# Kernel optimization log

Measured on AMD Instinct MI355X. Metric: run time of the kernel, lower is better.

## Reference

```python
import jax, jax.numpy as jnp
import numpy as np

N_NODES = 100000
D = 64


def sage_conv(x, src, dst, W_l, b_l, W_r, n_nodes):
    """PyG SAGEConv with mean aggregation and root_weight=True:
    out_i = lin_l(mean_{j in N(i)} x_j) + lin_r(x_i)
    Aggregation happens on raw features (as in PyG), then linear transforms.
    """
    deg = jax.ops.segment_sum(jnp.ones_like(dst, dtype=x.dtype), dst, num_segments=n_nodes)
    aggr = jax.ops.segment_sum(x[src], dst, num_segments=n_nodes)  # [N, D] gather-scatter
    aggr = aggr / jnp.maximum(deg, 1.0)[:, None]                    # mean (0 for isolated nodes)
    return aggr @ W_l.T + b_l + x @ W_r.T


def setup_inputs() -> dict:
    key = jax.random.key(0)
    k_x, k_e, k1, k2, k3, k4 = jax.random.split(key, 6)
    x = jax.random.normal(k_x, (N_NODES, D), dtype=jnp.float32)
    edge_index = jax.random.randint(k_e, (2, 1600000), 0, N_NODES, dtype=jnp.int64)
    s = 1.0 / np.sqrt(D)
    # layer 1 (SAGEConv: lin_l has bias, lin_r has no bias)
    W1_l = jax.random.uniform(k1, (D, D), jnp.float32, -s, s)
    b1_l = jnp.zeros((D,), jnp.float32)
    W1_r = jax.random.uniform(k2, (D, D), jnp.float32, -s, s)
    # layer 2
    W2_l = jax.random.uniform(k3, (D, D), jnp.float32, -s, s)
    b2_l = jnp.zeros((D,), jnp.float32)
    W2_r = jax.random.uniform(k4, (D, D), jnp.float32, -s, s)
    return {"x": x, "edge_index": edge_index,
            "W1_l": W1_l, "b1_l": b1_l, "W1_r": W1_r,
            "W2_l": W2_l, "b2_l": b2_l, "W2_r": W2_r}


def reference(x, edge_index, W1_l, b1_l, W1_r, W2_l, b2_l, W2_r):
    src, dst = edge_index[0], edge_index[1]
    n = x.shape[0]
    x1 = sage_conv(x, src, dst, W1_l, b1_l, W1_r, n)
    x2 = sage_conv(x1, src, dst, W2_l, b2_l, W2_r, n)
    return x2
```

## Files before the change

### kernel.cpp

```cpp
#include <hip/hip_runtime.h>

#define DD 64
#define BSHIFT 7
#define NBUCK_MAX 800
#define SEGCAP 4096
#define CBLK 512
#define SBLK 256

typedef unsigned short ushort_t;
typedef __attribute__((ext_vector_type(8))) short bf16x8;
typedef __attribute__((ext_vector_type(4))) short bf16x4;
typedef __attribute__((ext_vector_type(4))) float f32x4;

static __device__ __forceinline__ unsigned short f2bf(float f)
{
    unsigned u = __float_as_uint(f);
    unsigned r = (u + 0x7FFFu + ((u >> 16) & 1u)) >> 16;
    return (unsigned short)r;
}
static __device__ __forceinline__ float bf_lo(unsigned w) { return __uint_as_float(w << 16); }
static __device__ __forceinline__ float bf_hi(unsigned w) { return __uint_as_float(w & 0xFFFF0000u); }


__global__ __launch_bounds__(256)
void bucket_count(const int* __restrict__ dst, int* __restrict__ partialCnt,
                  int nE, int chunk, int nbuck)
{
    __shared__ int bins[NBUCK_MAX];
    int blk = blockIdx.x, t = threadIdx.x;
    for (int i = t; i < nbuck; i += 256) bins[i] = 0;
    __syncthreads();
    int e0 = blk * chunk;
    int e1 = e0 + chunk; if (e1 > nE) e1 = nE;
    for (int e = e0 + t; e < e1; e += 256)
        atomicAdd(&bins[dst[e] >> BSHIFT], 1);
    __syncthreads();
    for (int i = t; i < nbuck; i += 256)
        partialCnt[(size_t)i * CBLK + blk] = bins[i];
}

__global__ __launch_bounds__(CBLK)
void bucket_scanblocks(int* __restrict__ partialCnt, int* __restrict__ bucketTot)
{
    __shared__ int s[CBLK];
    int b = blockIdx.x, t = threadIdx.x;
    int v = partialCnt[(size_t)b * CBLK + t];
    s[t] = v;
    __syncthreads();
    for (int off = 1; off < CBLK; off <<= 1) {
        int u = (t >= off) ? s[t - off] : 0;
        __syncthreads();
        s[t] += u;
        __syncthreads();
    }
    partialCnt[(size_t)b * CBLK + t] = s[t] - v;
    if (t == CBLK - 1) bucketTot[b] = s[CBLK - 1];
}

__global__ __launch_bounds__(1024)
void bucket_scanbase(const int* __restrict__ bucketTot, int* __restrict__ bucketBase,
                     int* __restrict__ rs, int nbuck, int nN)
{
    __shared__ int s[1024];
    int t = threadIdx.x;
    int v = (t < nbuck) ? bucketTot[t] : 0;
    s[t] = v;
    __syncthreads();
    for (int off = 1; off < 1024; off <<= 1) {
        int u = (t >= off) ? s[t - off] : 0;
        __syncthreads();
        s[t] += u;
        __syncthreads();
    }
    if (t < nbuck) bucketBase[t] = s[t] - v;
    if (t == nbuck - 1) {
        bucketBase[nbuck] = s[t];
        rs[nN] = s[t];
    }
}

__global__ __launch_bounds__(256)
void bucket_scatter(const int* __restrict__ src, const int* __restrict__ dst,
                    const int* __restrict__ partialCnt,
                    const int* __restrict__ bucketBase,
                    int* __restrict__ buckEdges, int nE, int chunk, int nbuck)
{
    __shared__ int bins[NBUCK_MAX];
    __shared__ int wOff[NBUCK_MAX];
    int blk = blockIdx.x, t = threadIdx.x;
    for (int i = t; i < nbuck; i += 256) {
        bins[i] = 0;
        wOff[i] = bucketBase[i] + partialCnt[(size_t)i * CBLK + 2 * blk];
    }
    __syncthreads();
    int e0 = blk * chunk;
    int e1 = e0 + chunk; if (e1 > nE) e1 = nE;
    for (int e = e0 + t; e < e1; e += 256) {
        int d = dst[e];
        int sv = src[e];
        int bb = d >> BSHIFT;
        int r = atomicAdd(&bins[bb], 1);
        buckEdges[wOff[bb] + r] = sv | ((d & 127) << 17);
    }
}

__global__ __launch_bounds__(256)
void bucket_finalize(const int* __restrict__ buckEdges,
                     const int* __restrict__ bucketBase,
                     int* __restrict__ rs, int* __restrict__ csr,
                     float* __restrict__ indf, int nN)
{
    __shared__ int eLds[SEGCAP];
    __shared__ int segLds[SEGCAP];
    __shared__ int deg[128];
    __shared__ int basec[128];
    __shared__ int cur[128];
    int b = blockIdx.x, t = threadIdx.x;
    int e0 = bucketBase[b], e1 = bucketBase[b + 1];
    int nb = e1 - e0;
    bool staged = (nb <= SEGCAP);
    if (t < 128) deg[t] = 0;
    __syncthreads();
    for (int i = t; i < nb; i += 256) {
        int p = buckEdges[e0 + i];
        if (staged) eLds[i] = p;
        atomicAdd(&deg[(p >> 17) & 127], 1);
    }
    __syncthreads();
    if (t < 128) basec[t] = deg[t];
    __syncthreads();
    for (int off = 1; off < 128; off <<= 1) {
        int u = 0;
        if (t < 128 && t >= off) u = basec[t - off];
        __syncthreads();
        if (t < 128) basec[t] += u;
        __syncthreads();
    }
    int nodeBase = b << BSHIFT;
    if (t < 128) {
        int node = nodeBase + t;
        int ex = basec[t] - deg[t];
        if (node < nN) {
            rs[node] = e0 + ex;
            indf[node] = deg[t] > 0 ? 1.0f : 0.0f;
        }
        cur[t] = ex;
    }
    __syncthreads();
    for (int i = t; i < nb; i += 256) {
        int p = staged ? eLds[i] : buckEdges[e0 + i];
        int dl = (p >> 17) & 127;
        int slot = atomicAdd(&cur[dl], 1);
        int sv = p & 0x1FFFF;
        if (staged) segLds[slot] = sv;
        else        csr[e0 + slot] = sv;
    }
    __syncthreads();
    if (staged)
        for (int i = t; i < nb; i += 256)
            csr[e0 + i] = segLds[i];
}

__global__ __launch_bounds__(256)
void tobf16_kernel(const float* __restrict__ in, ushort_t* __restrict__ outh,
                   int nTot8)
{
    int i = blockIdx.x * 256 + threadIdx.x;
    if (i >= nTot8) return;
    float4 v0 = *(const float4*)(in + (size_t)i * 8);
    float4 v1 = *(const float4*)(in + (size_t)i * 8 + 4);
    uint4 o;
    o.x = (unsigned)f2bf(v0.x) | ((unsigned)f2bf(v0.y) << 16);
    o.y = (unsigned)f2bf(v0.z) | ((unsigned)f2bf(v0.w) << 16);
    o.z = (unsigned)f2bf(v1.x) | ((unsigned)f2bf(v1.y) << 16);
    o.w = (unsigned)f2bf(v1.z) | ((unsigned)f2bf(v1.w) << 16);
    *(uint4*)(outh + (size_t)i * 8) = o;
}

__global__ void prep_kernel(const float* __restrict__ W1l,
                            const float* __restrict__ W1r,
                            const float* __restrict__ W2l,
                            const float* __restrict__ W2r,
                            const float* __restrict__ b1,
                            const float* __restrict__ b2,
                            float* __restrict__ MT1, float* __restrict__ MT2,
                            float* __restrict__ MT3, float* __restrict__ c0,
                            float* __restrict__ c1)
{
    int f = blockIdx.x;
    int k = threadIdx.x;
    float m1 = 0.f, m2 = 0.f, m3 = 0.f;
    for (int j = 0; j < DD; ++j) {
        float a2l = W2l[f * DD + j];
        float a2r = W2r[f * DD + j];
        float w1l = W1l[j * DD + k];
        float w1r = W1r[j * DD + k];
        m1 = fmaf(a2l, w1l, m1);
        m2 = fmaf(a2l, w1r, m2);
        m2 = fmaf(a2r, w1l, m2);
        m3 = fmaf(a2r, w1r, m3);
    }
    MT1[k * DD + f] = m1;
    MT2[k * DD + f] = m2;
    MT3[k * DD + f] = m3;
    float t1 = W2l[f * DD + k] * b1[k];
    float t0 = W2r[f * DD + k] * b1[k];
    for (int off = 1; off < 64; off <<= 1) {
        t1 += __shfl_xor(t1, off);
        t0 += __shfl_xor(t0, off);
    }
    if (k == 0) {
        c1[f] = t1;
        c0[f] = t0 + b2[f];
    }
}

__global__ __launch_bounds__(256)
void pack_weights(const float* __restrict__ MT1, const float* __restrict__ MT2,
                  const float* __restrict__ MT3, ushort_t* __restrict__ Wp)
{
    int idx = blockIdx.x * 256 + threadIdx.x;
    if (idx >= 12288) return;
    int e    = idx & 7;
    int lane = (idx >> 3) & 63;
    int ft   = (idx >> 9) & 3;
    int kt   = (idx >> 11) & 1;
    int m    = idx >> 12;
    int kin  = ((lane >> 4) * 4) + (e & 3) + 16 * (e >> 2);
    int gk   = kt * 32 + kin;
    int f    = ft * 16 + (lane & 15);
    const float* MT = (m == 0) ? MT1 : (m == 1) ? MT2 : MT3;
    Wp[idx] = f2bf(MT[gk * DD + f]);
}

__global__ __launch_bounds__(256, 4)
void aggregate_bf16g(const ushort_t* __restrict__ xh,
                     const int* __restrict__ csr,
                     const int* __restrict__ rs,
                     ushort_t* __restrict__ aggrh, int nN)
{
    int lane = threadIdx.x & 63;
    int w = threadIdx.x >> 6;
    int g  = lane >> 3;
    int gl = lane & 7;
    int node = (blockIdx.x * 4 + w) * 8 + g;
    int valid = node < nN;
    int nd = valid ? node : nN - 1;
    int beg = rs[nd], end = rs[nd + 1];
    int deg = end - beg;

    float4 aL0 = {0,0,0,0}, aH0 = {0,0,0,0};
    float4 aL1 = {0,0,0,0}, aH1 = {0,0,0,0};
    float4 aL2 = {0,0,0,0}, aH2 = {0,0,0,0};
    float4 aL3 = {0,0,0,0}, aH3 = {0,0,0,0};

#define ROWA(S, L, H)                                                         \
    {                                                                         \
        uint4 v = *(const uint4*)(xh + (size_t)(S) * DD + gl * 8);            \
        L.x += bf_lo(v.x); L.y += bf_hi(v.x);                                 \
        L.z += bf_lo(v.y); L.w += bf_hi(v.y);                                 \
        H.x += bf_lo(v.z); H.y += bf_hi(v.z);                                 \
        H.z += bf_lo(v.w); H.w += bf_hi(v.w);                                 \
    }
#define ROWM(S, MM, L, H)                                                     \
    {                                                                         \
        uint4 v = *(const uint4*)(xh + (size_t)(S) * DD + gl * 8);            \
        L.x = fmaf(MM, bf_lo(v.x), L.x); L.y = fmaf(MM, bf_hi(v.x), L.y);     \
        L.z = fmaf(MM, bf_lo(v.y), L.z); L.w = fmaf(MM, bf_hi(v.y), L.w);     \
        H.x = fmaf(MM, bf_lo(v.z), H.x); H.y = fmaf(MM, bf_hi(v.z), H.y);     \
        H.z = fmaf(MM, bf_lo(v.w), H.z); H.w = fmaf(MM, bf_hi(v.w), H.w);     \
    }

    for (int ch = 0; ch < deg; ch += 8) {
        int ii = ch + gl;
        int myIdx = csr[(ii < deg) ? (beg + ii) : beg];
        int lb = g << 3;
        if (ch + 8 <= deg) {
            int s0 = __shfl(myIdx, lb + 0);
            int s1 = __shfl(myIdx, lb + 1);
            int s2 = __shfl(myIdx, lb + 2);
            int s3 = __shfl(myIdx, lb + 3);
            ROWA(s0, aL0, aH0) ROWA(s1, aL1, aH1)
            ROWA(s2, aL2, aH2) ROWA(s3, aL3, aH3)
            int s4 = __shfl(myIdx, lb + 4);
            int s5 = __shfl(myIdx, lb + 5);
            int s6 = __shfl(myIdx, lb + 6);
            int s7 = __shfl(myIdx, lb + 7);
            ROWA(s4, aL0, aH0) ROWA(s5, aL1, aH1)
            ROWA(s6, aL2, aH2) ROWA(s7, aL3, aH3)
        } else {
            int rem = deg - ch;
            int s0 = __shfl(myIdx, lb + 0);
            int s1 = __shfl(myIdx, lb + 1);
            int s2 = __shfl(myIdx, lb + 2);
            int s3 = __shfl(myIdx, lb + 3);
            float m0 = (0 < rem) ? 1.f : 0.f;
            float m1 = (1 < rem) ? 1.f : 0.f;
            float m2 = (2 < rem) ? 1.f : 0.f;
            float m3 = (3 < rem) ? 1.f : 0.f;
            ROWM(s0, m0, aL0, aH0) ROWM(s1, m1, aL1, aH1)
            ROWM(s2, m2, aL2, aH2) ROWM(s3, m3, aL3, aH3)
            int s4 = __shfl(myIdx, lb + 4);
            int s5 = __shfl(myIdx, lb + 5);
            int s6 = __shfl(myIdx, lb + 6);
            int s7 = __shfl(myIdx, lb + 7);
            float m4 = (4 < rem) ? 1.f : 0.f;
            float m5 = (5 < rem) ? 1.f : 0.f;
            float m6 = (6 < rem) ? 1.f : 0.f;
            float m7 = (7 < rem) ? 1.f : 0.f;
            ROWM(s4, m4, aL0, aH0) ROWM(s5, m5, aL1, aH1)
            ROWM(s6, m6, aL2, aH2) ROWM(s7, m7, aL3, aH3)
        }
    }
#undef ROWA
#undef ROWM

    float4 L, H;
    L.x = (aL0.x + aL1.x) + (aL2.x + aL3.x);
    L.y = (aL0.y + aL1.y) + (aL2.y + aL3.y);
    L.z = (aL0.z + aL1.z) + (aL2.z + aL3.z);
    L.w = (aL0.w + aL1.w) + (aL2.w + aL3.w);
    H.x = (aH0.x + aH1.x) + (aH2.x + aH3.x);
    H.y = (aH0.y + aH1.y) + (aH2.y + aH3.y);
    H.z = (aH0.z + aH1.z) + (aH2.z + aH3.z);
    H.w = (aH0.w + aH1.w) + (aH2.w + aH3.w);
    if (valid) {
        float inv = 1.0f / (float)(deg > 0 ? deg : 1);
        uint4 o;
        o.x = (unsigned)f2bf(L.x * inv) | ((unsigned)f2bf(L.y * inv) << 16);
        o.y = (unsigned)f2bf(L.z * inv) | ((unsigned)f2bf(L.w * inv) << 16);
        o.z = (unsigned)f2bf(H.x * inv) | ((unsigned)f2bf(H.y * inv) << 16);
        o.w = (unsigned)f2bf(H.z * inv) | ((unsigned)f2bf(H.w * inv) << 16);
        *(uint4*)(aggrh + (size_t)node * DD + gl * 8) = o;
    }
}

__global__ __launch_bounds__(256)
void tri_dense_mfma(const ushort_t* __restrict__ agg2h,
                    const ushort_t* __restrict__ agg1h,
                    const ushort_t* __restrict__ xh,
                    const ushort_t* __restrict__ Wp,
                    const float* __restrict__ c0,
                    const float* __restrict__ c1,
                    const float* __restrict__ indf,
                    float* __restrict__ out, int nN)
{
    int lane = threadIdx.x & 63;
    int w = threadIdx.x >> 6;
    int base = (blockIdx.x * 4 + w) * 16;
    if (base >= nN) return;
    int mrow = lane & 15;
    int kg   = lane >> 4;
    size_t rowoff = (size_t)(base + mrow) * DD + kg * 4;

    bf16x4 aLo[3][2], aHi[3][2];
#pragma unroll
    for (int m = 0; m < 3; ++m) {
        const ushort_t* sp = (m == 0) ? agg2h : (m == 1) ? agg1h : xh;
#pragma unroll
        for (int kt = 0; kt < 2; ++kt) {
            aLo[m][kt] = *(const bf16x4*)(sp + rowoff + kt * 32);
            aHi[m][kt] = *(const bf16x4*)(sp + rowoff + kt * 32 + 16);
        }
    }
    float ind0 = indf[base + kg * 4 + 0];
    float ind1 = indf[base + kg * 4 + 1];
    float ind2 = indf[base + kg * 4 + 2];
    float ind3 = indf[base + kg * 4 + 3];
    float c0v[4], c1v[4];
#pragma unroll
    for (int ft = 0; ft < 4; ++ft) {
        c0v[ft] = c0[ft * 16 + mrow];
        c1v[ft] = c1[ft * 16 + mrow];
    }

    f32x4 acc0 = {0,0,0,0}, acc1 = {0,0,0,0}, acc2 = {0,0,0,0}, acc3 = {0,0,0,0};
#pragma unroll
    for (int m = 0; m < 3; ++m) {
#pragma unroll
        for (int kt = 0; kt < 2; ++kt) {
            bf16x8 a;
            a[0] = aLo[m][kt][0]; a[1] = aLo[m][kt][1];
            a[2] = aLo[m][kt][2]; a[3] = aLo[m][kt][3];
            a[4] = aHi[m][kt][0]; a[5] = aHi[m][kt][1];
            a[6] = aHi[m][kt][2]; a[7] = aHi[m][kt][3];
            const ushort_t* wp = Wp + ((m * 2 + kt) * 4) * 512 + lane * 8;
            bf16x8 b0 = *(const bf16x8*)(wp);
            bf16x8 b1 = *(const bf16x8*)(wp + 512);
            bf16x8 b2 = *(const bf16x8*)(wp + 1024);
            bf16x8 b3 = *(const bf16x8*)(wp + 1536);
            acc0 = __builtin_amdgcn_mfma_f32_16x16x32_bf16(a, b0, acc0, 0, 0, 0);
            acc1 = __builtin_amdgcn_mfma_f32_16x16x32_bf16(a, b1, acc1, 0, 0, 0);
            acc2 = __builtin_amdgcn_mfma_f32_16x16x32_bf16(a, b2, acc2, 0, 0, 0);
            acc3 = __builtin_amdgcn_mfma_f32_16x16x32_bf16(a, b3, acc3, 0, 0, 0);
        }
    }

#define STORE_T(ACC, ft)                                                      \
    {                                                                         \
        int f = (ft) * 16 + mrow;                                             \
        size_t o = (size_t)(base + kg * 4) * DD + f;                          \
        out[o         ] = ACC[0] + c0v[ft] + ind0 * c1v[ft];                  \
        out[o + DD    ] = ACC[1] + c0v[ft] + ind1 * c1v[ft];                  \
        out[o + 2 * DD] = ACC[2] + c0v[ft] + ind2 * c1v[ft];                  \
        out[o + 3 * DD] = ACC[3] + c0v[ft] + ind3 * c1v[ft];                  \
    }
    STORE_T(acc0, 0) STORE_T(acc1, 1) STORE_T(acc2, 2) STORE_T(acc3, 3)
#undef STORE_T
}

extern "C" void kernel_launch(void* const* d_in, const int* in_sizes, int n_in,
                              void* d_out, int out_size, void* d_ws, size_t ws_size,
                              hipStream_t stream)
{
    const float* x   = (const float*)d_in[0];
    const int*   ei  = (const int*)d_in[1];
    const float* W1l = (const float*)d_in[2];
    const float* b1l = (const float*)d_in[3];
    const float* W1r = (const float*)d_in[4];
    const float* W2l = (const float*)d_in[5];
    const float* b2l = (const float*)d_in[6];
    const float* W2r = (const float*)d_in[7];
    float* out = (float*)d_out;

    int nN = in_sizes[0] / DD;
    int nE = in_sizes[1] / 2;
    const int* src = ei;
    const int* dst = ei + nE;

    int nbuck = (nN + 127) >> BSHIFT;
    int cchunk = (nE + CBLK - 1) / CBLK;
    int schunk = cchunk * 2;

    int* rs         = (int*)d_ws;
    int* partialCnt = rs + nN + 1;
    int* bucketTot  = partialCnt + (size_t)nbuck * CBLK;
    int* bucketBase = bucketTot + nbuck;
    int* csr        = bucketBase + nbuck + 1;
    int* buckEdges  = csr + nE;
    size_t ofs = (size_t)(buckEdges + nE - (int*)d_ws);
    ofs = (ofs + 3) & ~(size_t)3;
    float* MT1 = (float*)d_ws + ofs;
    float* MT2 = MT1 + DD * DD;
    float* MT3 = MT2 + DD * DD;
    float* c0 = MT3 + DD * DD;
    float* c1 = c0 + DD;
    float* xh_f    = c1 + DD;
    float* agg1h_f = xh_f + (size_t)nN * 32;
    float* agg2h_f = agg1h_f + (size_t)nN * 32;
    float* indf    = agg2h_f + (size_t)nN * 32;
    ushort_t* Wp   = (ushort_t*)(indf + nN);
    ushort_t* xh    = (ushort_t*)xh_f;
    ushort_t* agg1h = (ushort_t*)agg1h_f;
    ushort_t* agg2h = (ushort_t*)agg2h_f;

    int ncv  = (nN * 32 / 4 + 255) / 256;
    int nagg = (nN + 31) / 32;
    int nmf  = (nN / 16 + 3) / 4;

    bucket_count<<<CBLK, 256, 0, stream>>>(dst, partialCnt, nE, cchunk, nbuck);
    bucket_scanblocks<<<nbuck, CBLK, 0, stream>>>(partialCnt, bucketTot);
    bucket_scanbase<<<1, 1024, 0, stream>>>(bucketTot, bucketBase, rs, nbuck, nN);
    bucket_scatter<<<SBLK, 256, 0, stream>>>(src, dst, partialCnt, bucketBase,
                                             buckEdges, nE, schunk, nbuck);
    bucket_finalize<<<nbuck, 256, 0, stream>>>(buckEdges, bucketBase, rs, csr,
                                               indf, nN);

    prep_kernel<<<64, 64, 0, stream>>>(W1l, W1r, W2l, W2r, b1l, b2l,
                                       MT1, MT2, MT3, c0, c1);
    pack_weights<<<48, 256, 0, stream>>>(MT1, MT2, MT3, Wp);
    tobf16_kernel<<<ncv, 256, 0, stream>>>(x, xh, nN * DD / 8);

    aggregate_bf16g<<<nagg, 256, 0, stream>>>(xh, csr, rs, agg1h, nN);
    aggregate_bf16g<<<nagg, 256, 0, stream>>>(agg1h, csr, rs, agg2h, nN);

    tri_dense_mfma<<<nmf, 256, 0, stream>>>(agg2h, agg1h, xh, Wp,
                                            c0, c1, indf, out, nN);
}
```

Measured before the change: 141.7 us.

## Gather neighbor features in FP8 instead of BF16 for both aggregations

Node features are quantized to 8-bit floats before the edge gathers. Both aggregation passes now read 64-byte rows instead of 128-byte rows, roughly halving the random gather traffic. The first aggregation writes an FP8 copy alongside its BF16 output for the second pass to gather from. The dense MFMA stage reads the original fp32 x and converts it to BF16 in registers instead of using a BF16 copy. The cost is lower feature precision in the aggregated means, which risks accuracy against the fp32 reference, plus extra pack and convert work.

```diff
diff --git a/kernel.cpp b/kernel.cpp
--- a/kernel.cpp
+++ b/kernel.cpp
@@ -8,9 +8,20 @@
 #define SBLK 256
 
 typedef unsigned short ushort_t;
+typedef unsigned char uchar_t;
 typedef __attribute__((ext_vector_type(8))) short bf16x8;
 typedef __attribute__((ext_vector_type(4))) short bf16x4;
 typedef __attribute__((ext_vector_type(4))) float f32x4;
+typedef __attribute__((ext_vector_type(2))) float f32x2;
+
+#if defined(__has_builtin)
+#if __has_builtin(__builtin_amdgcn_cvt_pk_f32_fp8) && __has_builtin(__builtin_amdgcn_cvt_pk_fp8_f32)
+#define HW_FP8 1
+#endif
+#endif
+#ifndef HW_FP8
+#define HW_FP8 0
+#endif
 
 static __device__ __forceinline__ unsigned short f2bf(float f)
 {
@@ -20,6 +31,43 @@
 }
 static __device__ __forceinline__ float bf_lo(unsigned w) { return __uint_as_float(w << 16); }
 static __device__ __forceinline__ float bf_hi(unsigned w) { return __uint_as_float(w & 0xFFFF0000u); }
+
+static __device__ __forceinline__ unsigned f2q8_sw(float f)
+{
+    unsigned u = __float_as_uint(f);
+    unsigned s = (u >> 31) << 7;
+    unsigned um = __float_as_uint(__uint_as_float(u & 0x7FFFFFFFu) * 0x1.0p-120f);
+    unsigned q = (um + 0x7FFFFu + ((um >> 20) & 1u)) >> 20;
+    if (q > 0x7Eu) q = 0x7Eu;
+    return s | q;
+}
+static __device__ __forceinline__ float q2f_sw(unsigned b)
+{
+    unsigned u = ((b & 0x80u) << 24) | ((b & 0x7Fu) << 20);
+    return __uint_as_float(u) * 0x1.0p120f;
+}
+template<int WORD>
+static __device__ __forceinline__ f32x2 cvt2(unsigned u)
+{
+#if HW_FP8
+    return __builtin_amdgcn_cvt_pk_f32_fp8(u, WORD);
+#else
+    unsigned b0 = (u >> (WORD * 16)) & 0xFFu;
+    unsigned b1 = (u >> (WORD * 16 + 8)) & 0xFFu;
+    f32x2 r; r[0] = q2f_sw(b0); r[1] = q2f_sw(b1);
+    return r;
+#endif
+}
+template<int WORD>
+static __device__ __forceinline__ unsigned pk8(float x, float y, unsigned old)
+{
+#if HW_FP8
+    return __builtin_amdgcn_cvt_pk_fp8_f32(x, y, old, WORD);
+#else
+    unsigned q = f2q8_sw(x) | (f2q8_sw(y) << 8);
+    return WORD ? ((old & 0x0000FFFFu) | (q << 16)) : ((old & 0xFFFF0000u) | q);
+#endif
+}
 
 
 __global__ __launch_bounds__(256)
@@ -162,19 +210,19 @@
 }
 
 __global__ __launch_bounds__(256)
-void tobf16_kernel(const float* __restrict__ in, ushort_t* __restrict__ outh,
-                   int nTot8)
+void tofp8_kernel(const float* __restrict__ in, uchar_t* __restrict__ outq,
+                  int nTot8)
 {
     int i = blockIdx.x * 256 + threadIdx.x;
     if (i >= nTot8) return;
     float4 v0 = *(const float4*)(in + (size_t)i * 8);
     float4 v1 = *(const float4*)(in + (size_t)i * 8 + 4);
-    uint4 o;
-    o.x = (unsigned)f2bf(v0.x) | ((unsigned)f2bf(v0.y) << 16);
-    o.y = (unsigned)f2bf(v0.z) | ((unsigned)f2bf(v0.w) << 16);
-    o.z = (unsigned)f2bf(v1.x) | ((unsigned)f2bf(v1.y) << 16);
-    o.w = (unsigned)f2bf(v1.z) | ((unsigned)f2bf(v1.w) << 16);
-    *(uint4*)(outh + (size_t)i * 8) = o;
+    unsigned w0 = pk8<0>(v0.x, v0.y, 0u);
+    w0 = pk8<1>(v0.z, v0.w, w0);
+    unsigned w1 = pk8<0>(v1.x, v1.y, 0u);
+    w1 = pk8<1>(v1.z, v1.w, w1);
+    uint2 o; o.x = w0; o.y = w1;
+    *(uint2*)(outq + (size_t)i * 8) = o;
 }
 
 __global__ void prep_kernel(const float* __restrict__ W1l,
@@ -234,10 +282,12 @@
 }
 
 __global__ __launch_bounds__(256, 4)
-void aggregate_bf16g(const ushort_t* __restrict__ xh,
-                     const int* __restrict__ csr,
-                     const int* __restrict__ rs,
-                     ushort_t* __restrict__ aggrh, int nN)
+void aggregate_fp8(const uchar_t* __restrict__ xq,
+                   const int* __restrict__ csr,
+                   const int* __restrict__ rs,
+                   ushort_t* __restrict__ aggrh,
+                   uchar_t* __restrict__ aggrq,
+                   int nN)
 {
     int lane = threadIdx.x & 63;
     int w = threadIdx.x >> 6;
@@ -249,26 +299,28 @@
     int beg = rs[nd], end = rs[nd + 1];
     int deg = end - beg;
 
-    float4 aL0 = {0,0,0,0}, aH0 = {0,0,0,0};
-    float4 aL1 = {0,0,0,0}, aH1 = {0,0,0,0};
-    float4 aL2 = {0,0,0,0}, aH2 = {0,0,0,0};
-    float4 aL3 = {0,0,0,0}, aH3 = {0,0,0,0};
-
-#define ROWA(S, L, H)                                                         \
+    float4 A0 = {0,0,0,0}, B0 = {0,0,0,0};
+    float4 A1 = {0,0,0,0}, B1 = {0,0,0,0};
+    float4 A2 = {0,0,0,0}, B2 = {0,0,0,0};
+    float4 A3 = {0,0,0,0}, B3 = {0,0,0,0};
+
+#define ROWA(S, A, B)                                                         \
     {                                                                         \
-        uint4 v = *(const uint4*)(xh + (size_t)(S) * DD + gl * 8);            \
-        L.x += bf_lo(v.x); L.y += bf_hi(v.x);                                 \
-        L.z += bf_lo(v.y); L.w += bf_hi(v.y);                                 \
-        H.x += bf_lo(v.z); H.y += bf_hi(v.z);                                 \
-        H.z += bf_lo(v.w); H.w += bf_hi(v.w);                                 \
-    }
-#define ROWM(S, MM, L, H)                                                     \
+        uint2 v = *(const uint2*)(xq + (size_t)(S) * DD + gl * 8);            \
+        f32x2 f;                                                              \
+        f = cvt2<0>(v.x); A.x += f[0]; A.y += f[1];                           \
+        f = cvt2<1>(v.x); A.z += f[0]; A.w += f[1];                           \
+        f = cvt2<0>(v.y); B.x += f[0]; B.y += f[1];                           \
+        f = cvt2<1>(v.y); B.z += f[0]; B.w += f[1];                           \
+    }
+#define ROWM(S, MM, A, B)                                                     \
     {                                                                         \
-        uint4 v = *(const uint4*)(xh + (size_t)(S) * DD + gl * 8);            \
-        L.x = fmaf(MM, bf_lo(v.x), L.x); L.y = fmaf(MM, bf_hi(v.x), L.y);     \
-        L.z = fmaf(MM, bf_lo(v.y), L.z); L.w = fmaf(MM, bf_hi(v.y), L.w);     \
-        H.x = fmaf(MM, bf_lo(v.z), H.x); H.y = fmaf(MM, bf_hi(v.z), H.y);     \
-        H.z = fmaf(MM, bf_lo(v.w), H.z); H.w = fmaf(MM, bf_hi(v.w), H.w);     \
+        uint2 v = *(const uint2*)(xq + (size_t)(S) * DD + gl * 8);            \
+        f32x2 f;                                                              \
+        f = cvt2<0>(v.x); A.x = fmaf(MM, f[0], A.x); A.y = fmaf(MM, f[1], A.y); \
+        f = cvt2<1>(v.x); A.z = fmaf(MM, f[0], A.z); A.w = fmaf(MM, f[1], A.w); \
+        f = cvt2<0>(v.y); B.x = fmaf(MM, f[0], B.x); B.y = fmaf(MM, f[1], B.y); \
+        f = cvt2<1>(v.y); B.z = fmaf(MM, f[0], B.z); B.w = fmaf(MM, f[1], B.w); \
     }
 
     for (int ch = 0; ch < deg; ch += 8) {
@@ -280,14 +332,14 @@
             int s1 = __shfl(myIdx, lb + 1);
             int s2 = __shfl(myIdx, lb + 2);
             int s3 = __shfl(myIdx, lb + 3);
-            ROWA(s0, aL0, aH0) ROWA(s1, aL1, aH1)
-            ROWA(s2, aL2, aH2) ROWA(s3, aL3, aH3)
+            ROWA(s0, A0, B0) ROWA(s1, A1, B1)
+            ROWA(s2, A2, B2) ROWA(s3, A3, B3)
             int s4 = __shfl(myIdx, lb + 4);
             int s5 = __shfl(myIdx, lb + 5);
             int s6 = __shfl(myIdx, lb + 6);
             int s7 = __shfl(myIdx, lb + 7);
-            ROWA(s4, aL0, aH0) ROWA(s5, aL1, aH1)
-            ROWA(s6, aL2, aH2) ROWA(s7, aL3, aH3)
+            ROWA(s4, A0, B0) ROWA(s5, A1, B1)
+            ROWA(s6, A2, B2) ROWA(s7, A3, B3)
         } else {
             int rem = deg - ch;
             int s0 = __shfl(myIdx, lb + 0);
@@ -298,8 +350,8 @@
             float m1 = (1 < rem) ? 1.f : 0.f;
             float m2 = (2 < rem) ? 1.f : 0.f;
             float m3 = (3 < rem) ? 1.f : 0.f;
-            ROWM(s0, m0, aL0, aH0) ROWM(s1, m1, aL1, aH1)
-            ROWM(s2, m2, aL2, aH2) ROWM(s3, m3, aL3, aH3)
+            ROWM(s0, m0, A0, B0) ROWM(s1, m1, A1, B1)
+            ROWM(s2, m2, A2, B2) ROWM(s3, m3, A3, B3)
             int s4 = __shfl(myIdx, lb + 4);
             int s5 = __shfl(myIdx, lb + 5);
             int s6 = __shfl(myIdx, lb + 6);
@@ -308,37 +360,45 @@
             float m5 = (5 < rem) ? 1.f : 0.f;
             float m6 = (6 < rem) ? 1.f : 0.f;
             float m7 = (7 < rem) ? 1.f : 0.f;
-            ROWM(s4, m4, aL0, aH0) ROWM(s5, m5, aL1, aH1)
-            ROWM(s6, m6, aL2, aH2) ROWM(s7, m7, aL3, aH3)
+            ROWM(s4, m4, A0, B0) ROWM(s5, m5, A1, B1)
+            ROWM(s6, m6, A2, B2) ROWM(s7, m7, A3, B3)
         }
     }
 #undef ROWA
 #undef ROWM
 
-    float4 L, H;
-    L.x = (aL0.x + aL1.x) + (aL2.x + aL3.x);
-    L.y = (aL0.y + aL1.y) + (aL2.y + aL3.y);
-    L.z = (aL0.z + aL1.z) + (aL2.z + aL3.z);
-    L.w = (aL0.w + aL1.w) + (aL2.w + aL3.w);
-    H.x = (aH0.x + aH1.x) + (aH2.x + aH3.x);
-    H.y = (aH0.y + aH1.y) + (aH2.y + aH3.y);
-    H.z = (aH0.z + aH1.z) + (aH2.z + aH3.z);
-    H.w = (aH0.w + aH1.w) + (aH2.w + aH3.w);
     if (valid) {
         float inv = 1.0f / (float)(deg > 0 ? deg : 1);
+        float4 L, H;
+        L.x = ((A0.x + A1.x) + (A2.x + A3.x)) * inv;
+        L.y = ((A0.y + A1.y) + (A2.y + A3.y)) * inv;
+        L.z = ((A0.z + A1.z) + (A2.z + A3.z)) * inv;
+        L.w = ((A0.w + A1.w) + (A2.w + A3.w)) * inv;
+        H.x = ((B0.x + B1.x) + (B2.x + B3.x)) * inv;
+        H.y = ((B0.y + B1.y) + (B2.y + B3.y)) * inv;
+        H.z = ((B0.z + B1.z) + (B2.z + B3.z)) * inv;
+        H.w = ((B0.w + B1.w) + (B2.w + B3.w)) * inv;
         uint4 o;
-        o.x = (unsigned)f2bf(L.x * inv) | ((unsigned)f2bf(L.y * inv) << 16);
-        o.y = (unsigned)f2bf(L.z * inv) | ((unsigned)f2bf(L.w * inv) << 16);
-        o.z = (unsigned)f2bf(H.x * inv) | ((unsigned)f2bf(H.y * inv) << 16);
-        o.w = (unsigned)f2bf(H.z * inv) | ((unsigned)f2bf(H.w * inv) << 16);
+        o.x = (unsigned)f2bf(L.x) | ((unsigned)f2bf(L.y) << 16);
+        o.y = (unsigned)f2bf(L.z) | ((unsigned)f2bf(L.w) << 16);
+        o.z = (unsigned)f2bf(H.x) | ((unsigned)f2bf(H.y) << 16);
+        o.w = (unsigned)f2bf(H.z) | ((unsigned)f2bf(H.w) << 16);
         *(uint4*)(aggrh + (size_t)node * DD + gl * 8) = o;
+        if (aggrq) {
+            unsigned w0 = pk8<0>(L.x, L.y, 0u);
+            w0 = pk8<1>(L.z, L.w, w0);
+            unsigned w1 = pk8<0>(H.x, H.y, 0u);
+            w1 = pk8<1>(H.z, H.w, w1);
+            uint2 q; q.x = w0; q.y = w1;
+            *(uint2*)(aggrq + (size_t)node * DD + gl * 8) = q;
+        }
     }
 }
 
 __global__ __launch_bounds__(256)
 void tri_dense_mfma(const ushort_t* __restrict__ agg2h,
                     const ushort_t* __restrict__ agg1h,
-                    const ushort_t* __restrict__ xh,
+                    const float* __restrict__ xf,
                     const ushort_t* __restrict__ Wp,
                     const float* __restrict__ c0,
                     const float* __restrict__ c1,
@@ -353,15 +413,21 @@
     int kg   = lane >> 4;
     size_t rowoff = (size_t)(base + mrow) * DD + kg * 4;
 
-    bf16x4 aLo[3][2], aHi[3][2];
+    bf16x4 aLo[2][2], aHi[2][2];
 #pragma unroll
-    for (int m = 0; m < 3; ++m) {
-        const ushort_t* sp = (m == 0) ? agg2h : (m == 1) ? agg1h : xh;
+    for (int m = 0; m < 2; ++m) {
+        const ushort_t* sp = (m == 0) ? agg2h : agg1h;
 #pragma unroll
         for (int kt = 0; kt < 2; ++kt) {
             aLo[m][kt] = *(const bf16x4*)(sp + rowoff + kt * 32);
             aHi[m][kt] = *(const bf16x4*)(sp + rowoff + kt * 32 + 16);
         }
+    }
+    float4 xlo[2], xhi[2];
+#pragma unroll
+    for (int kt = 0; kt < 2; ++kt) {
+        xlo[kt] = *(const float4*)(xf + rowoff + kt * 32);
+        xhi[kt] = *(const float4*)(xf + rowoff + kt * 32 + 16);
     }
     float ind0 = indf[base + kg * 4 + 0];
     float ind1 = indf[base + kg * 4 + 1];
@@ -380,10 +446,17 @@
 #pragma unroll
         for (int kt = 0; kt < 2; ++kt) {
             bf16x8 a;
-            a[0] = aLo[m][kt][0]; a[1] = aLo[m][kt][1];
-            a[2] = aLo[m][kt][2]; a[3] = aLo[m][kt][3];
-            a[4] = aHi[m][kt][0]; a[5] = aHi[m][kt][1];
-            a[6] = aHi[m][kt][2]; a[7] = aHi[m][kt][3];
+            if (m < 2) {
+                a[0] = aLo[m][kt][0]; a[1] = aLo[m][kt][1];
+                a[2] = aLo[m][kt][2]; a[3] = aLo[m][kt][3];
+                a[4] = aHi[m][kt][0]; a[5] = aHi[m][kt][1];
+                a[6] = aHi[m][kt][2]; a[7] = aHi[m][kt][3];
+            } else {
+                a[0] = (short)f2bf(xlo[kt].x); a[1] = (short)f2bf(xlo[kt].y);
+                a[2] = (short)f2bf(xlo[kt].z); a[3] = (short)f2bf(xlo[kt].w);
+                a[4] = (short)f2bf(xhi[kt].x); a[5] = (short)f2bf(xhi[kt].y);
+                a[6] = (short)f2bf(xhi[kt].z); a[7] = (short)f2bf(xhi[kt].w);
+            }
             const ushort_t* wp = Wp + ((m * 2 + kt) * 4) * 512 + lane * 8;
             bf16x8 b0 = *(const bf16x8*)(wp);
             bf16x8 b1 = *(const bf16x8*)(wp + 512);
@@ -438,6 +511,7 @@
     int* bucketBase = bucketTot + nbuck;
     int* csr        = bucketBase + nbuck + 1;
     int* buckEdges  = csr + nE;
+    uchar_t* xq     = (uchar_t*)buckEdges;
     size_t ofs = (size_t)(buckEdges + nE - (int*)d_ws);
     ofs = (ofs + 3) & ~(size_t)3;
     float* MT1 = (float*)d_ws + ofs;
@@ -445,16 +519,16 @@
     float* MT3 = MT2 + DD * DD;
     float* c0 = MT3 + DD * DD;
     float* c1 = c0 + DD;
-    float* xh_f    = c1 + DD;
-    float* agg1h_f = xh_f + (size_t)nN * 32;
+    float* agg1h_f = c1 + DD;
     float* agg2h_f = agg1h_f + (size_t)nN * 32;
-    float* indf    = agg2h_f + (size_t)nN * 32;
+    float* agg1q_f = agg2h_f + (size_t)nN * 32;
+    float* indf    = agg1q_f + (size_t)nN * 16;
     ushort_t* Wp   = (ushort_t*)(indf + nN);
-    ushort_t* xh    = (ushort_t*)xh_f;
     ushort_t* agg1h = (ushort_t*)agg1h_f;
     ushort_t* agg2h = (ushort_t*)agg2h_f;
-
-    int ncv  = (nN * 32 / 4 + 255) / 256;
+    uchar_t*  agg1q = (uchar_t*)agg1q_f;
+
+    int ncv  = (nN * 8 + 255) / 256;
     int nagg = (nN + 31) / 32;
     int nmf  = (nN / 16 + 3) / 4;
 
@@ -469,11 +543,12 @@
     prep_kernel<<<64, 64, 0, stream>>>(W1l, W1r, W2l, W2r, b1l, b2l,
                                        MT1, MT2, MT3, c0, c1);
     pack_weights<<<48, 256, 0, stream>>>(MT1, MT2, MT3, Wp);
-    tobf16_kernel<<<ncv, 256, 0, stream>>>(x, xh, nN * DD / 8);
-
-    aggregate_bf16g<<<nagg, 256, 0, stream>>>(xh, csr, rs, agg1h, nN);
-    aggregate_bf16g<<<nagg, 256, 0, stream>>>(agg1h, csr, rs, agg2h, nN);
-
-    tri_dense_mfma<<<nmf, 256, 0, stream>>>(agg2h, agg1h, xh, Wp,
+    tofp8_kernel<<<ncv, 256, 0, stream>>>(x, xq, nN * 8);
+
+    aggregate_fp8<<<nagg, 256, 0, stream>>>(xq, csr, rs, agg1h, agg1q, nN);
+    aggregate_fp8<<<nagg, 256, 0, stream>>>(agg1q, csr, rs, agg2h,
+                                            (uchar_t*)nullptr, nN);
+
+    tri_dense_mfma<<<nmf, 256, 0, stream>>>(agg2h, agg1h, x, Wp,
                                             c0, c1, indf, out, nN);
 }
```

Measured after the change: 134.2 us. -5.3%, faster.
